# Performance work log

Measured on AMD Instinct MI355X. Metric: run time of the kernel, lower is better.

Reference implementation:

```python
import jax, jax.numpy as jnp
import numpy as np

N_NODES = 100000
N_EDGES = 1600000
N_GRAPHS = 128
IN_DIM, HID, OUT_DIM, DOC_DIM = 64, 128, 32, 768
LAYERS = 3


def setup_inputs() -> dict:
    key = jax.random.key(0)
    ks = jax.random.split(key, 24)
    s = 0.05
    inp = {
        "x": jax.random.normal(ks[0], (N_NODES, IN_DIM), jnp.float32),
        "doc_features": jax.random.normal(ks[1], (N_GRAPHS, DOC_DIM), jnp.float32),
        "edge_index": jax.random.randint(ks[2], (2, N_EDGES), 0, N_NODES, jnp.int64),
        "batch": jnp.sort(jax.random.randint(ks[3], (N_NODES,), 0, N_GRAPHS, jnp.int64)),
        # parameters (stored as [in, out] so y = x @ W + b)
        "node_w": jax.random.normal(ks[4], (IN_DIM, HID), jnp.float32) * s,
        "node_b": jnp.zeros((HID,), jnp.float32),
        "ggnn_w": jax.random.normal(ks[5], (LAYERS, HID, HID), jnp.float32) * s,
        "gru_w_ih": jax.random.normal(ks[6], (HID, 3 * HID), jnp.float32) * s,
        "gru_b_ih": jnp.zeros((3 * HID,), jnp.float32),
        "gru_w_hh": jax.random.normal(ks[7], (HID, 3 * HID), jnp.float32) * s,
        "gru_b_hh": jnp.zeros((3 * HID,), jnp.float32),
        "doc_w": jax.random.normal(ks[8], (DOC_DIM, HID), jnp.float32) * s,
        "doc_b": jnp.zeros((HID,), jnp.float32),
        "ln_g": jnp.ones((2 * HID,), jnp.float32),
        "ln_b": jnp.zeros((2 * HID,), jnp.float32),
        "fus_w": jax.random.normal(ks[9], (2 * HID, HID), jnp.float32) * s,
        "fus_b": jnp.zeros((HID,), jnp.float32),
        "task_w": jax.random.normal(ks[10], (HID, OUT_DIM), jnp.float32) * s,
        "task_b": jnp.zeros((OUT_DIM,), jnp.float32),
        "time_w": jax.random.normal(ks[11], (HID, 1), jnp.float32) * s,
        "time_b": jnp.zeros((1,), jnp.float32),
    }
    return inp


def _gru(m, h, w_ih, b_ih, w_hh, b_hh):
    gi = m @ w_ih + b_ih  # [N, 3H]
    gh = h @ w_hh + b_hh
    ir, iz, in_ = jnp.split(gi, 3, axis=-1)
    hr, hz, hn = jnp.split(gh, 3, axis=-1)
    r = jax.nn.sigmoid(ir + hr)
    z = jax.nn.sigmoid(iz + hz)
    n = jnp.tanh(in_ + r * hn)
    return (1.0 - z) * n + z * h


def reference(x, doc_features, node_w, node_b, ggnn_w, gru_w_ih, gru_b_ih,
              gru_w_hh, gru_b_hh, doc_w, doc_b, ln_g, ln_b, fus_w, fus_b,
              task_w, task_b, time_w, time_b, edge_index, batch):
    N = x.shape[0]
    src, dst = edge_index[0], edge_index[1]
    # node projection + ReLU
    h = jax.nn.relu(x @ node_w + node_b)  # [N, H]
    # GatedGraphConv: 3 layers of (linear -> scatter-add over edges -> GRU)
    for i in range(LAYERS):
        m = h @ ggnn_w[i]                              # [N, H]
        agg = jax.ops.segment_sum(m[src], dst, num_segments=N)  # scatter-add
        h = _gru(agg, h, gru_w_ih, gru_b_ih, gru_w_hh, gru_b_hh)
    # global mean pool over graphs
    sums = jax.ops.segment_sum(h, batch, num_segments=N_GRAPHS)  # [G, H]
    cnt = jax.ops.segment_sum(jnp.ones((N,), h.dtype), batch, num_segments=N_GRAPHS)
    pooled = sums / jnp.maximum(cnt, 1.0)[:, None]
    # doc projection + fusion head
    doc_emb = jax.nn.relu(doc_features @ doc_w + doc_b)  # [G, H]
    fusion = jnp.concatenate([pooled, doc_emb], axis=1)  # [G, 2H]
    mu = jnp.mean(fusion, axis=-1, keepdims=True)
    var = jnp.mean(jnp.square(fusion - mu), axis=-1, keepdims=True)
    fusion = (fusion - mu) * jax.lax.rsqrt(var + 1e-5) * ln_g + ln_b
    fusion = jax.nn.relu(fusion @ fus_w + fus_b)  # dropout is identity (eval)
    task_output = fusion @ task_w + task_b
    time_output = fusion @ time_w + time_b
    return (task_output, time_output)
```

## Files before the change

### kernel.cpp

```cpp
#include <hip/hip_runtime.h>

#define N_NODES  100000
#define N_EDGES  1600000
#define N_GRAPHS 128

#define BSH      8
#define BNODES   (1 << BSH)
#define NBUCK    391
#define NBLK_P1  512
#define EPB      (N_EDGES / NBLK_P1)
#define BKT_SCAN_N   (NBUCK * NBLK_P1)
#define SCAN_BLK_BKT 196
#define SCAN_BLK_NODE 98

typedef unsigned short u16;
typedef unsigned int   u32;
typedef __attribute__((ext_vector_type(8))) short short8;
typedef __attribute__((ext_vector_type(4))) float f32x4;

__device__ __forceinline__ float bf2f(u16 v) {
  union { u32 i; float f; } u; u.i = ((u32)v) << 16; return u.f;
}
__device__ __forceinline__ u16 f2bf(float f) {
  union { float f; u32 i; } u; u.f = f;
  u32 r = (u.i + 0x7fffu + ((u.i >> 16) & 1u)) >> 16;
  return (u16)r;
}
__device__ __forceinline__ float sigmoid_f(float x) { return 1.f / (1.f + __expf(-x)); }
__device__ __forceinline__ float tanh_f(float x) {
  x = fminf(15.f, fmaxf(-15.f, x));
  float e = __expf(2.f * x);
  return (e - 1.f) / (e + 1.f);
}
__device__ __forceinline__ int geti(const int* __restrict__ p, int i, int is64) {
  return p[is64 ? (2 * i) : i];
}

__global__ void detect_i64_kernel(const int* __restrict__ ei, const int* __restrict__ batch,
                                  int* __restrict__ flags) {
  int lane = threadIdx.x;
  {
    long long q = (long long)lane * (3200000 / 2 - 1) / 63;
    int pos = (int)(2 * q + 1);
    unsigned long long m = __ballot(ei[pos] != 0);
    if (lane == 0) flags[0] = (m == 0ull) ? 1 : 0;
  }
  {
    long long q = (long long)lane * (100000 / 2 - 1) / 63;
    int pos = (int)(2 * q + 1);
    unsigned long long m = __ballot(batch[pos] != 0);
    if (lane == 0) flags[1] = (m == 0ull) ? 1 : 0;
  }
}


__global__ __launch_bounds__(256)
void bucket_hist(const int* __restrict__ ei, const int* __restrict__ flags,
                 int* __restrict__ bcounts) {
  __shared__ int h[NBUCK];
  const int f = flags[0];
  for (int b = threadIdx.x; b < NBUCK; b += 256) h[b] = 0;
  __syncthreads();
  const int e0 = blockIdx.x * EPB;
  for (int i = threadIdx.x; i < EPB; i += 256) {
    int d = geti(ei, N_EDGES + e0 + i, f);
    atomicAdd(&h[d >> BSH], 1);
  }
  __syncthreads();
  for (int b = threadIdx.x; b < NBUCK; b += 256)
    bcounts[b * NBLK_P1 + blockIdx.x] = h[b];
}

__global__ __launch_bounds__(256)
void bucket_scatter(const int* __restrict__ ei, const int* __restrict__ flags,
                    const int* __restrict__ bbases, u32* __restrict__ bedges) {
  __shared__ int cur[NBUCK];
  const int f = flags[0];
  for (int b = threadIdx.x; b < NBUCK; b += 256)
    cur[b] = bbases[b * NBLK_P1 + blockIdx.x];
  __syncthreads();
  const int e0 = blockIdx.x * EPB;
  for (int i = threadIdx.x; i < EPB; i += 256) {
    int e = e0 + i;
    int d = geti(ei, N_EDGES + e, f);
    int s = geti(ei, e, f);
    int pos = atomicAdd(&cur[d >> BSH], 1);
    bedges[pos] = ((u32)(d & (BNODES - 1)) << 17) | (u32)s;
  }
}

__global__ __launch_bounds__(256)
void node_count(const u32* __restrict__ bedges, const int* __restrict__ bbases,
                int* __restrict__ counts) {
  __shared__ int h[BNODES];
  const int b = blockIdx.x;
  for (int i = threadIdx.x; i < BNODES; i += 256) h[i] = 0;
  __syncthreads();
  const int beg = bbases[b * NBLK_P1];
  const int end = (b + 1 < NBUCK) ? bbases[(b + 1) * NBLK_P1] : N_EDGES;
  for (int e = beg + threadIdx.x; e < end; e += 256)
    atomicAdd(&h[bedges[e] >> 17], 1);
  __syncthreads();
  const int node0 = b << BSH;
  for (int i = threadIdx.x; i < BNODES; i += 256)
    if (node0 + i < N_NODES) counts[node0 + i] = h[i];
}

__global__ __launch_bounds__(256)
void final_scatter(const u32* __restrict__ bedges, const int* __restrict__ bbases,
                   const int* __restrict__ offs, int* __restrict__ ssrc) {
  __shared__ int cur[BNODES];
  const int b = blockIdx.x;
  const int node0 = b << BSH;
  for (int i = threadIdx.x; i < BNODES; i += 256)
    cur[i] = (node0 + i < N_NODES) ? offs[node0 + i] : 0;
  __syncthreads();
  const int beg = bbases[b * NBLK_P1];
  const int end = (b + 1 < NBUCK) ? bbases[(b + 1) * NBLK_P1] : N_EDGES;
  for (int e = beg + threadIdx.x; e < end; e += 256) {
    u32 v = bedges[e];
    int pos = atomicAdd(&cur[v >> 17], 1);
    ssrc[pos] = (int)(v & 0x1FFFFu);
  }
}

__global__ __launch_bounds__(1024)
void scanA_kernel(const int* __restrict__ counts, int n, int* __restrict__ blocksums) {
  __shared__ int red[16];
  int i = blockIdx.x * 1024 + threadIdx.x;
  int v = (i < n) ? counts[i] : 0;
  for (int o = 32; o > 0; o >>= 1) v += __shfl_down(v, o, 64);
  int wv = threadIdx.x >> 6, lane = threadIdx.x & 63;
  if (lane == 0) red[wv] = v;
  __syncthreads();
  if (threadIdx.x < 16) {
    int s = red[threadIdx.x];
    for (int o = 8; o > 0; o >>= 1) s += __shfl_down(s, o, 64);
    if (threadIdx.x == 0) blocksums[blockIdx.x] = s;
  }
}

__global__ void scanB_kernel(const int* __restrict__ blocksums, int nblocks,
                             int* __restrict__ blockbase, int* __restrict__ total_out) {
  if (threadIdx.x == 0) {
    int run = 0;
    for (int b = 0; b < nblocks; ++b) { blockbase[b] = run; run += blocksums[b]; }
    if (total_out) *total_out = run;
  }
}

__global__ __launch_bounds__(1024)
void scanC_kernel(const int* __restrict__ counts, int n, const int* __restrict__ blockbase,
                  int* __restrict__ offsets) {
  __shared__ int buf[1024];
  int t = threadIdx.x;
  int i = blockIdx.x * 1024 + t;
  int v = (i < n) ? counts[i] : 0;
  buf[t] = v;
  __syncthreads();
  for (int o = 1; o < 1024; o <<= 1) {
    int add = (t >= o) ? buf[t - o] : 0;
    __syncthreads();
    buf[t] += add;
    __syncthreads();
  }
  if (i < n) offsets[i] = buf[t] - v + blockbase[blockIdx.x];
}

__global__ void transpose_kernel(const float* __restrict__ in, u16* __restrict__ out, int K, int N) {
  int i = blockIdx.x * 256 + threadIdx.x;
  if (i < K * N) {
    int k = i / N, n = i % N;
    out[n * K + k] = f2bf(in[i]);
  }
}

__global__ void wprime_kernel(const float* __restrict__ ggnn_w, const float* __restrict__ w_ih,
                              float* __restrict__ wp) {
  int i = blockIdx.x * 256 + threadIdx.x;
  if (i >= 3 * 128 * 384) return;
  int l = i / (128 * 384), r = i % (128 * 384), k = r / 384, c = r % 384;
  const float* W = ggnn_w + l * 128 * 128;
  float s = 0.f;
  for (int j = 0; j < 128; ++j) s += W[k * 128 + j] * w_ih[j * 384 + c];
  wp[i] = s;
}

__global__ void build_b2q_kernel(const float* __restrict__ wp, const float* __restrict__ w_hh,
                                 u16* __restrict__ b2q) {
  int g = blockIdx.x * 256 + threadIdx.x;
  if (g >= 98304) return;
  int r = g;
  int e    = r & 7;  r >>= 3;
  int quad = r & 3;  r >>= 2;
  int col  = r & 15; r >>= 4;
  int gate = r % 3;  r /= 3;
  int ci4  = r & 3;  r >>= 2;
  int half = r & 1;  r >>= 1;
  int oc   = r;
  int k = half * 128 + ci4 * 32 + quad * 8 + e;
  int n_lin = gate * 128 + oc * 16 + col;
  float v = (k < 128) ? wp[k * 384 + n_lin] : w_hh[(k - 128) * 384 + n_lin];
  b2q[g] = f2bf(v);
}

__global__ __launch_bounds__(256)
void nodeproj_gemm(const float* __restrict__ A, const u16* __restrict__ BT,
                   const float* __restrict__ bias, u16* __restrict__ out, int M)
{
  constexpr int K_DIM = 64, N_DIM = 128, NT = 8, NCHUNK = 2;
  __shared__ u16 B_lds[N_DIM * 40];
  const int tid = threadIdx.x, lane = tid & 63, w = tid >> 6;
  const int strip = blockIdx.x * 64;
  const int ksub = (lane >> 4) * 8;
  union Frag { uint4 u; short8 s; };
  Frag af[NCHUNK];
  const int m_node = strip + w * 16 + (lane & 15);
  const bool avalid = (m_node < M);
#pragma unroll
  for (int ci = 0; ci < NCHUNK; ++ci) {
    int k0 = ci * 32 + ksub;
    short8 sv = {0,0,0,0,0,0,0,0};
    if (avalid) {
      const float* p = A + (size_t)m_node * K_DIM + k0;
      float4 f0 = *(const float4*)p;
      float4 f1 = *(const float4*)(p + 4);
      sv[0]=(short)f2bf(f0.x); sv[1]=(short)f2bf(f0.y); sv[2]=(short)f2bf(f0.z); sv[3]=(short)f2bf(f0.w);
      sv[4]=(short)f2bf(f1.x); sv[5]=(short)f2bf(f1.y); sv[6]=(short)f2bf(f1.z); sv[7]=(short)f2bf(f1.w);
    }
    af[ci].s = sv;
  }
  f32x4 acc[NT];
#pragma unroll
  for (int t = 0; t < NT; ++t) acc[t] = {0.f, 0.f, 0.f, 0.f};
  const int boff = (lane & 15) * 40 + ksub;
#pragma unroll
  for (int ci = 0; ci < NCHUNK; ++ci) {
    if (ci) __syncthreads();
    for (int g = tid; g < N_DIM * 4; g += 256) {
      int n = g >> 2, ko = g & 3;
      uint4 bv = *(const uint4*)(BT + (size_t)n * K_DIM + ci * 32 + ko * 8);
      *(uint4*)(&B_lds[n * 40 + ko * 8]) = bv;
    }
    __syncthreads();
    short8 a = af[ci].s;
#pragma unroll
    for (int t = 0; t < NT; ++t) {
      const short8 b = *(const short8*)(&B_lds[t * 16 * 40 + boff]);
      acc[t] = __builtin_amdgcn_mfma_f32_16x16x32_bf16(a, b, acc[t], 0, 0, 0);
    }
  }
  const int mrow = (lane >> 4) * 4;
#pragma unroll
  for (int t = 0; t < NT; ++t) {
    int col = t * 16 + (lane & 15);
    float bv = bias[col];
#pragma unroll
    for (int r = 0; r < 4; ++r) {
      int node = strip + w * 16 + mrow + r;
      if (node < M) out[(size_t)node * N_DIM + col] = f2bf(fmaxf(acc[t][r] + bv, 0.f));
    }
  }
}

__global__ __launch_bounds__(256, 8)
void gru_gemm(const u16* __restrict__ agg, const u16* __restrict__ h,
              const u16* __restrict__ b2q, const float* __restrict__ b_ih,
              const float* __restrict__ b_hh, u16* __restrict__ hout, int M)
{
  __shared__ u16 Blds[6144];
  const int tid  = threadIdx.x;
  const int lane = tid & 63;
  const int w    = tid >> 6;
  const int bid  = blockIdx.x;
  const int linear = (bid & 7) * 1563 + (bid >> 3);
  const int oc   = linear & 7;
  const int strip = (linear >> 3) * 64;
  const int lrow = lane & 15;
  const int quad = lane >> 4;

  const int node = strip + w * 16 + lrow;
  const bool nv = (node < M);
  const u16* qsrc = b2q + (size_t)oc * 12288;

  union Frag { uint4 u; short8 s8; };
  Frag a[2];
  const uint4 zz = {0u, 0u, 0u, 0u};
  auto lda = [&](int ci, int p) {
    const u16* ap = (ci < 4) ? (agg + ci * 32 + quad * 8) : (h + (ci - 4) * 32 + quad * 8);
    a[p].u = nv ? *(const uint4*)(ap + (size_t)node * 128) : zz;
  };

  lda(0, 0);
  lda(1, 1);
  for (int idx = tid; idx < 768; idx += 256)
    *(uint4*)(&Blds[idx * 8]) = *(const uint4*)(qsrc + idx * 8);

  f32x4 ar = {0.f,0.f,0.f,0.f}, az = {0.f,0.f,0.f,0.f};
  f32x4 ain = {0.f,0.f,0.f,0.f}, ahn = {0.f,0.f,0.f,0.f};

  __syncthreads();

#pragma unroll
  for (int ci = 0; ci < 8; ++ci) {
    if (ci == 4) {
      __syncthreads();
      for (int idx = tid; idx < 768; idx += 256)
        *(uint4*)(&Blds[idx * 8]) = *(const uint4*)(qsrc + 6144 + idx * 8);
      __syncthreads();
    }
    const int p = ci & 1;
    const u16* lb = &Blds[(ci & 3) * 1536 + lrow * 32 + quad * 8];
    short8 br = *(const short8*)(lb);
    short8 bz = *(const short8*)(lb + 512);
    short8 bg = *(const short8*)(lb + 1024);
    short8 A = a[p].s8;
    if (ci < 6) lda(ci + 2, p);

    ar = __builtin_amdgcn_mfma_f32_16x16x32_bf16(A, br, ar, 0, 0, 0);
    az = __builtin_amdgcn_mfma_f32_16x16x32_bf16(A, bz, az, 0, 0, 0);
    if (ci < 4) ain = __builtin_amdgcn_mfma_f32_16x16x32_bf16(A, bg, ain, 0, 0, 0);
    else        ahn = __builtin_amdgcn_mfma_f32_16x16x32_bf16(A, bg, ahn, 0, 0, 0);
  }

  const int c = oc * 16 + lrow;
  const float brr = b_ih[c] + b_hh[c];
  const float bzz = b_ih[128 + c] + b_hh[128 + c];
  const float bin = b_ih[256 + c];
  const float bhn = b_hh[256 + c];
#pragma unroll
  for (int r = 0; r < 4; ++r) {
    const int nrow = strip + w * 16 + quad * 4 + r;
    if (nrow < M) {
      float rg = sigmoid_f(ar[r] + brr);
      float zg = sigmoid_f(az[r] + bzz);
      float hv = ahn[r] + bhn;
      float ng = tanh_f(ain[r] + bin + rg * hv);
      float hp = bf2f(h[(size_t)nrow * 128 + c]);
      hout[(size_t)nrow * 128 + c] = f2bf((1.f - zg) * ng + zg * hp);
    }
  }
}

__global__ __launch_bounds__(256)
void agg_kernel(const u16* __restrict__ m, const int* __restrict__ ssrc,
                const int* __restrict__ offsets, u16* __restrict__ agg)
{
  int node = blockIdx.x * 4 + (threadIdx.x >> 6);
  int lane = threadIdx.x & 63;
  if (node >= N_NODES) return;
  const int g = lane >> 4, l = lane & 15;
  int beg = offsets[node], end = offsets[node + 1];
  float s[8] = {0.f,0.f,0.f,0.f,0.f,0.f,0.f,0.f};
  for (int e = beg; e < end; e += 8) {
    uint4 v0 = {0u,0u,0u,0u}, v1 = {0u,0u,0u,0u};
    int e0 = e + g, e1 = e + 4 + g;
    if (e0 < end) { int src = ssrc[e0]; v0 = *(const uint4*)(m + (size_t)src * 128 + l * 8); }
    if (e1 < end) { int src = ssrc[e1]; v1 = *(const uint4*)(m + (size_t)src * 128 + l * 8); }
    u32 w0[4] = {v0.x, v0.y, v0.z, v0.w};
    u32 w1[4] = {v1.x, v1.y, v1.z, v1.w};
#pragma unroll
    for (int i = 0; i < 4; ++i) {
      s[2*i]   += bf2f((u16)(w0[i] & 0xffffu)) + bf2f((u16)(w1[i] & 0xffffu));
      s[2*i+1] += bf2f((u16)(w0[i] >> 16))     + bf2f((u16)(w1[i] >> 16));
    }
  }
#pragma unroll
  for (int i = 0; i < 8; ++i) {
    s[i] += __shfl_xor(s[i], 16, 64);
    s[i] += __shfl_xor(s[i], 32, 64);
  }
  if (g == 0) {
    uint4 o;
    o.x = (u32)f2bf(s[0]) | ((u32)f2bf(s[1]) << 16);
    o.y = (u32)f2bf(s[2]) | ((u32)f2bf(s[3]) << 16);
    o.z = (u32)f2bf(s[4]) | ((u32)f2bf(s[5]) << 16);
    o.w = (u32)f2bf(s[6]) | ((u32)f2bf(s[7]) << 16);
    *(uint4*)(agg + (size_t)node * 128 + l * 8) = o;
  }
}

__global__ __launch_bounds__(256)
void pool_kernel(const u16* __restrict__ h, const int* __restrict__ batch,
                 const int* __restrict__ flags, float* __restrict__ sums)
{
  const int c = threadIdx.x & 127;
  const int half = threadIdx.x >> 7;
  const int base = blockIdx.x * 128;
  const int f = flags[1];
  int gcur = -1; float s = 0.f;
  for (int i = half; i < 128; i += 2) {
    int n = base + i;
    if (n >= N_NODES) break;
    int g = geti(batch, n, f);
    if (g != gcur) {
      if (gcur >= 0) atomicAdd(&sums[gcur * 128 + c], s);
      s = 0.f; gcur = g;
    }
    s += bf2f(h[(size_t)n * 128 + c]);
  }
  if (gcur >= 0) atomicAdd(&sums[gcur * 128 + c], s);
}

__global__ __launch_bounds__(256)
void head2_kernel(const float* __restrict__ sums, const int* __restrict__ batch,
                  const int* __restrict__ flags,
                  const float* __restrict__ doc, const float* __restrict__ doc_w, const float* __restrict__ doc_b,
                  const float* __restrict__ ln_g, const float* __restrict__ ln_b,
                  const float* __restrict__ fus_w, const float* __restrict__ fus_b,
                  const float* __restrict__ task_w, const float* __restrict__ task_b,
                  const float* __restrict__ time_w, const float* __restrict__ time_b,
                  float* __restrict__ out_task, float* __restrict__ out_time)
{
  const int g = blockIdx.x;
  const int t = threadIdx.x;
  __shared__ float fusion[256];
  __shared__ float fh[128];
  __shared__ float dpart[256];
  __shared__ int seg[2];

  if (t < 2) {
    int f = flags[1];
    int target = g + t, lo = 0, hi = N_NODES;
    while (lo < hi) { int mid = (lo + hi) >> 1; if (geti(batch, mid, f) < target) lo = mid + 1; else hi = mid; }
    seg[t] = lo;
  }
  {
    int c = t & 127, kh = t >> 7;
    float s = 0.f;
    for (int k = kh * 384; k < kh * 384 + 384; ++k) s += doc[g * 768 + k] * doc_w[k * 128 + c];
    dpart[t] = s;
  }
  __syncthreads();

  if (t < 128) {
    float cnt = (float)(seg[1] - seg[0]);
    fusion[t] = sums[g * 128 + t] / fmaxf(cnt, 1.f);
  } else {
    int c = t - 128;
    fusion[t] = fmaxf(dpart[c] + dpart[c + 128] + doc_b[c], 0.f);
  }
  __syncthreads();

  float mu = 0.f;
  for (int i = 0; i < 256; ++i) mu += fusion[i];
  mu *= (1.f / 256.f);
  float var = 0.f;
  for (int i = 0; i < 256; ++i) { float d = fusion[i] - mu; var += d * d; }
  var *= (1.f / 256.f);
  float inv = rsqrtf(var + 1e-5f);
  float norm = (fusion[t] - mu) * inv * ln_g[t] + ln_b[t];
  __syncthreads();
  fusion[t] = norm;
  __syncthreads();

  if (t < 128) {
    float s = 0.f;
    for (int k = 0; k < 256; ++k) s += fusion[k] * fus_w[k * 128 + t];
    s += fus_b[t];
    fh[t] = fmaxf(s, 0.f);
  }
  __syncthreads();

  if (t < 32) {
    float s = 0.f;
    for (int k = 0; k < 128; ++k) s += fh[k] * task_w[k * 32 + t];
    s += task_b[t];
    out_task[g * 32 + t] = s;
  }
  if (t == 32) {
    float s = 0.f;
    for (int k = 0; k < 128; ++k) s += fh[k] * time_w[k];
    s += time_b[0];
    out_time[g] = s;
  }
}

extern "C" void kernel_launch(void* const* d_in, const int* in_sizes, int n_in,
                              void* d_out, int out_size, void* d_ws, size_t ws_size,
                              hipStream_t stream)
{
  const float* x        = (const float*)d_in[0];
  const float* doc      = (const float*)d_in[1];
  const int*   ei       = (const int*)d_in[2];
  const int*   batch    = (const int*)d_in[3];
  const float* node_w   = (const float*)d_in[4];
  const float* node_b   = (const float*)d_in[5];
  const float* ggnn_w   = (const float*)d_in[6];
  const float* gru_w_ih = (const float*)d_in[7];
  const float* gru_b_ih = (const float*)d_in[8];
  const float* gru_w_hh = (const float*)d_in[9];
  const float* gru_b_hh = (const float*)d_in[10];
  const float* doc_w    = (const float*)d_in[11];
  const float* doc_b    = (const float*)d_in[12];
  const float* ln_g     = (const float*)d_in[13];
  const float* ln_b     = (const float*)d_in[14];
  const float* fus_w    = (const float*)d_in[15];
  const float* fus_b    = (const float*)d_in[16];
  const float* task_w   = (const float*)d_in[17];
  const float* task_b   = (const float*)d_in[18];
  const float* time_w   = (const float*)d_in[19];
  const float* time_b   = (const float*)d_in[20];

  char* ws = (char*)d_ws;
  size_t off = 0;
  auto alloc = [&](size_t bytes) -> void* {
    void* p = ws + off;
    off = (off + bytes + 255) & ~(size_t)255;
    return p;
  };
  u16* aggb    = (u16*)alloc((size_t)N_NODES * 128 * 2);
  u16* hA      = (u16*)alloc((size_t)N_NODES * 128 * 2);
  u16* hB      = (u16*)alloc((size_t)N_NODES * 128 * 2);
  u16* nwT     = (u16*)alloc(64 * 128 * 2);
  u16* b2q     = (u16*)alloc(3 * 98304 * 2);
  float* wp    = (float*)alloc(3 * 128 * 384 * 4);
  float* sums  = (float*)alloc(N_GRAPHS * 128 * 4);
  int* counts  = (int*)alloc((size_t)N_NODES * 4);
  int* offs    = (int*)alloc((size_t)(N_NODES + 1) * 4);
  int* ssrc    = (int*)alloc((size_t)N_EDGES * 4);
  int* bsum    = (int*)alloc(SCAN_BLK_BKT * 4);
  int* bbase   = (int*)alloc(SCAN_BLK_BKT * 4);
  int* flags   = (int*)alloc(2 * 4);

  u32* bedges  = (u32*)aggb;
  int* bcounts = (int*)((char*)aggb + 6400000);
  int* bbases  = (int*)((char*)aggb + 7200768);

  hipMemsetAsync(sums, 0, (size_t)N_GRAPHS * 128 * 4, stream);

  detect_i64_kernel<<<1, 64, 0, stream>>>(ei, batch, flags);

  bucket_hist<<<NBLK_P1, 256, 0, stream>>>(ei, flags, bcounts);
  scanA_kernel<<<SCAN_BLK_BKT, 1024, 0, stream>>>(bcounts, BKT_SCAN_N, bsum);
  scanB_kernel<<<1, 64, 0, stream>>>(bsum, SCAN_BLK_BKT, bbase, (int*)nullptr);
  scanC_kernel<<<SCAN_BLK_BKT, 1024, 0, stream>>>(bcounts, BKT_SCAN_N, bbase, bbases);
  bucket_scatter<<<NBLK_P1, 256, 0, stream>>>(ei, flags, bbases, bedges);
  node_count<<<NBUCK, 256, 0, stream>>>(bedges, bbases, counts);
  scanA_kernel<<<SCAN_BLK_NODE, 1024, 0, stream>>>(counts, N_NODES, bsum);
  scanB_kernel<<<1, 64, 0, stream>>>(bsum, SCAN_BLK_NODE, bbase, offs + N_NODES);
  scanC_kernel<<<SCAN_BLK_NODE, 1024, 0, stream>>>(counts, N_NODES, bbase, offs);
  final_scatter<<<NBUCK, 256, 0, stream>>>(bedges, bbases, offs, ssrc);

  transpose_kernel<<<(64 * 128 + 255) / 256, 256, 0, stream>>>(node_w, nwT, 64, 128);
  wprime_kernel<<<(3 * 128 * 384 + 255) / 256, 256, 0, stream>>>(ggnn_w, gru_w_ih, wp);
  for (int l = 0; l < 3; ++l)
    build_b2q_kernel<<<(98304 + 255) / 256, 256, 0, stream>>>(
        wp + l * 128 * 384, gru_w_hh, b2q + (size_t)l * 98304);

  const int GB = (N_NODES + 63) / 64;
  const int GBGRU = ((N_NODES + 63) / 64) * 8;
  nodeproj_gemm<<<GB, 256, 0, stream>>>(x, nwT, node_b, hA, N_NODES);

  u16* hcur = hA;
  u16* hnext = hB;
  for (int l = 0; l < 3; ++l) {
    agg_kernel<<<(N_NODES + 3) / 4, 256, 0, stream>>>(hcur, ssrc, offs, aggb);
    gru_gemm<<<GBGRU, 256, 0, stream>>>(aggb, hcur, b2q + (size_t)l * 98304,
                                        gru_b_ih, gru_b_hh, hnext, N_NODES);
    u16* tmp = hcur; hcur = hnext; hnext = tmp;
  }

  pool_kernel<<<(N_NODES + 127) / 128, 256, 0, stream>>>(hcur, batch, flags, sums);

  float* out_task = (float*)d_out;
  float* out_time = out_task + N_GRAPHS * 32;
  head2_kernel<<<N_GRAPHS, 256, 0, stream>>>(sums, batch, flags, doc, doc_w, doc_b, ln_g, ln_b,
                                             fus_w, fus_b, task_w, task_b, time_w, time_b,
                                             out_task, out_time);
}
```

Baseline: 672.1 us.

## Widen GRU GEMM tiles to two column groups and stage output through LDS

Each gru_gemm block now computes 32 output columns (two 16-column groups) instead of 16, so every A fragment loaded from agg and h feeds twice as many MFMAs and the grid shrinks by half. The B layout in build_b2q is reordered to match a new LDS read pattern. Results are staged in LDS so each thread writes one 16-byte global store instead of scattered 2-byte stores, and the XCD block remap is adjusted for the new grid. The cost is double the LDS use and more live accumulators, with the occupancy hint lowered from 8 to 6 blocks.

```diff
diff --git a/kernel.cpp b/kernel.cpp
--- a/kernel.cpp
+++ b/kernel.cpp
@@ -192,8 +192,8 @@
   if (g >= 98304) return;
   int r = g;
   int e    = r & 7;  r >>= 3;
+  int col  = r & 15; r >>= 4;
   int quad = r & 3;  r >>= 2;
-  int col  = r & 15; r >>= 4;
   int gate = r % 3;  r /= 3;
   int ci4  = r & 3;  r >>= 2;
   int half = r & 1;  r >>= 1;
@@ -263,25 +263,27 @@
   }
 }
 
-__global__ __launch_bounds__(256, 8)
+__global__ __launch_bounds__(256, 6)
 void gru_gemm(const u16* __restrict__ agg, const u16* __restrict__ h,
               const u16* __restrict__ b2q, const float* __restrict__ b_ih,
               const float* __restrict__ b_hh, u16* __restrict__ hout, int M)
 {
-  __shared__ u16 Blds[6144];
+  __shared__ u16 Blds[12288];
   const int tid  = threadIdx.x;
   const int lane = tid & 63;
   const int w    = tid >> 6;
   const int bid  = blockIdx.x;
-  const int linear = (bid & 7) * 1563 + (bid >> 3);
-  const int oc   = linear & 7;
-  const int strip = (linear >> 3) * 64;
+  const int xcd = bid & 7, idx = bid >> 3;
+  const int linear = ((xcd < 4) ? xcd * 782 : 4 * 782 + (xcd - 4) * 781) + idx;
+  const int op    = linear & 3;
+  const int strip = (linear >> 2) * 64;
   const int lrow = lane & 15;
   const int quad = lane >> 4;
 
   const int node = strip + w * 16 + lrow;
   const bool nv = (node < M);
-  const u16* qsrc = b2q + (size_t)oc * 12288;
+  const u16* qsrc0 = b2q + (size_t)(op * 2)     * 12288;
+  const u16* qsrc1 = b2q + (size_t)(op * 2 + 1) * 12288;
 
   union Frag { uint4 u; short8 s8; };
   Frag a[2];
@@ -293,11 +295,17 @@
 
   lda(0, 0);
   lda(1, 1);
-  for (int idx = tid; idx < 768; idx += 256)
-    *(uint4*)(&Blds[idx * 8]) = *(const uint4*)(qsrc + idx * 8);
-
-  f32x4 ar = {0.f,0.f,0.f,0.f}, az = {0.f,0.f,0.f,0.f};
-  f32x4 ain = {0.f,0.f,0.f,0.f}, ahn = {0.f,0.f,0.f,0.f};
+  for (int i2 = tid; i2 < 768; i2 += 256) {
+    *(uint4*)(&Blds[i2 * 8])        = *(const uint4*)(qsrc0 + i2 * 8);
+    *(uint4*)(&Blds[6144 + i2 * 8]) = *(const uint4*)(qsrc1 + i2 * 8);
+  }
+
+  f32x4 ar[2], az[2], ain[2], ahn[2];
+#pragma unroll
+  for (int t = 0; t < 2; ++t) {
+    ar[t] = {0.f,0.f,0.f,0.f}; az[t] = {0.f,0.f,0.f,0.f};
+    ain[t] = {0.f,0.f,0.f,0.f}; ahn[t] = {0.f,0.f,0.f,0.f};
+  }
 
   __syncthreads();
 
@@ -305,40 +313,60 @@
   for (int ci = 0; ci < 8; ++ci) {
     if (ci == 4) {
       __syncthreads();
-      for (int idx = tid; idx < 768; idx += 256)
-        *(uint4*)(&Blds[idx * 8]) = *(const uint4*)(qsrc + 6144 + idx * 8);
+      for (int i2 = tid; i2 < 768; i2 += 256) {
+        *(uint4*)(&Blds[i2 * 8])        = *(const uint4*)(qsrc0 + 6144 + i2 * 8);
+        *(uint4*)(&Blds[6144 + i2 * 8]) = *(const uint4*)(qsrc1 + 6144 + i2 * 8);
+      }
       __syncthreads();
     }
     const int p = ci & 1;
-    const u16* lb = &Blds[(ci & 3) * 1536 + lrow * 32 + quad * 8];
-    short8 br = *(const short8*)(lb);
-    short8 bz = *(const short8*)(lb + 512);
-    short8 bg = *(const short8*)(lb + 1024);
     short8 A = a[p].s8;
     if (ci < 6) lda(ci + 2, p);
-
-    ar = __builtin_amdgcn_mfma_f32_16x16x32_bf16(A, br, ar, 0, 0, 0);
-    az = __builtin_amdgcn_mfma_f32_16x16x32_bf16(A, bz, az, 0, 0, 0);
-    if (ci < 4) ain = __builtin_amdgcn_mfma_f32_16x16x32_bf16(A, bg, ain, 0, 0, 0);
-    else        ahn = __builtin_amdgcn_mfma_f32_16x16x32_bf16(A, bg, ahn, 0, 0, 0);
-  }
-
-  const int c = oc * 16 + lrow;
-  const float brr = b_ih[c] + b_hh[c];
-  const float bzz = b_ih[128 + c] + b_hh[128 + c];
-  const float bin = b_ih[256 + c];
-  const float bhn = b_hh[256 + c];
-#pragma unroll
-  for (int r = 0; r < 4; ++r) {
-    const int nrow = strip + w * 16 + quad * 4 + r;
-    if (nrow < M) {
-      float rg = sigmoid_f(ar[r] + brr);
-      float zg = sigmoid_f(az[r] + bzz);
-      float hv = ahn[r] + bhn;
-      float ng = tanh_f(ain[r] + bin + rg * hv);
-      float hp = bf2f(h[(size_t)nrow * 128 + c]);
-      hout[(size_t)nrow * 128 + c] = f2bf((1.f - zg) * ng + zg * hp);
-    }
+#pragma unroll
+    for (int t = 0; t < 2; ++t) {
+      const u16* lb = &Blds[t * 6144 + (ci & 3) * 1536 + quad * 128 + lrow * 8];
+      short8 br = *(const short8*)(lb);
+      short8 bz = *(const short8*)(lb + 512);
+      short8 bg = *(const short8*)(lb + 1024);
+      ar[t] = __builtin_amdgcn_mfma_f32_16x16x32_bf16(A, br, ar[t], 0, 0, 0);
+      az[t] = __builtin_amdgcn_mfma_f32_16x16x32_bf16(A, bz, az[t], 0, 0, 0);
+      if (ci < 4) ain[t] = __builtin_amdgcn_mfma_f32_16x16x32_bf16(A, bg, ain[t], 0, 0, 0);
+      else        ahn[t] = __builtin_amdgcn_mfma_f32_16x16x32_bf16(A, bg, ahn[t], 0, 0, 0);
+    }
+  }
+
+  __syncthreads();
+  u16* Olds = (u16*)Blds;
+#pragma unroll
+  for (int t = 0; t < 2; ++t) {
+    const int c = op * 32 + t * 16 + lrow;
+    const float brr = b_ih[c] + b_hh[c];
+    const float bzz = b_ih[128 + c] + b_hh[128 + c];
+    const float bin = b_ih[256 + c];
+    const float bhn = b_hh[256 + c];
+#pragma unroll
+    for (int r = 0; r < 4; ++r) {
+      const int lr   = w * 16 + quad * 4 + r;
+      const int nrow = strip + lr;
+      u16 val = 0;
+      if (nrow < M) {
+        float rg = sigmoid_f(ar[t][r] + brr);
+        float zg = sigmoid_f(az[t][r] + bzz);
+        float hv = ahn[t][r] + bhn;
+        float ng = tanh_f(ain[t][r] + bin + rg * hv);
+        float hp = bf2f(h[(size_t)nrow * 128 + c]);
+        val = f2bf((1.f - zg) * ng + zg * hp);
+      }
+      Olds[lr * 32 + t * 16 + lrow] = val;
+    }
+  }
+  __syncthreads();
+  {
+    const int row = tid >> 2, c4 = tid & 3;
+    const int nrow = strip + row;
+    if (nrow < M)
+      *(uint4*)(&hout[(size_t)nrow * 128 + op * 32 + c4 * 8]) =
+          *(const uint4*)(&Olds[row * 32 + c4 * 8]);
   }
 }
 
@@ -549,7 +577,7 @@
         wp + l * 128 * 384, gru_w_hh, b2q + (size_t)l * 98304);
 
   const int GB = (N_NODES + 63) / 64;
-  const int GBGRU = ((N_NODES + 63) / 64) * 8;
+  const int GBGRU = ((N_NODES + 63) / 64) * 4;
   nodeproj_gemm<<<GB, 256, 0, stream>>>(x, nwT, node_b, hA, N_NODES);
 
   u16* hcur = hA;
```

Measured after the change: 604.1 us, median of 2. -10.1%, faster.
